# Optimization experiments

Measured on AMD Instinct MI355X. Metric: run time of the kernel, lower is better.

Reference implementation:

```python
import jax, jax.numpy as jnp
import numpy as np

GRID_SIZE = 64
THRESHOLD = 1.0
SIGMA = 1.5
K_SHARP = 2.0


def _gaussian_kernel(sigma):
    ksize = max(int(4 * sigma) | 1, 3)
    x = jnp.arange(ksize, dtype=jnp.float32) - ksize // 2
    g1d = jnp.exp(-x ** 2 / (2.0 * sigma ** 2))
    g2d = g1d[None, :] * g1d[:, None]
    g2d = g2d / g2d.sum()
    return g2d[None, None]  # (1,1,k,k) OIHW


def setup_inputs() -> dict:
    key = jax.random.key(0)
    k1, k2, k3, k4 = jax.random.split(key, 4)
    B, V, P, N, MAXP = 4, 512, 8192, 2000, 8
    positions = jax.random.uniform(k1, (B, V, 2), dtype=jnp.float32) * 2.0 - 1.0
    pin_offsets = jax.random.normal(k2, (P, 2), dtype=jnp.float32) * 0.05
    net_to_pin = jax.random.randint(k3, (N, MAXP), 0, P, dtype=jnp.int32)
    pin_to_macro = jax.random.randint(k4, (P,), 0, V, dtype=jnp.int32)
    return {"positions": positions, "pin_offsets": pin_offsets,
            "net_to_pin": net_to_pin, "pin_to_macro": pin_to_macro}


def reference(positions, pin_offsets, net_to_pin, pin_to_macro):
    B = positions.shape[0]
    M = GRID_SIZE
    num_nets = net_to_pin.shape[0]

    # pin positions: (B, P, 2) -- no rotation (rotation_onehot=None branch)
    pin_pos = positions[:, pin_to_macro, :] + pin_offsets[None]

    # per-net bounding boxes over valid pins
    valid = net_to_pin >= 0                                  # (N, maxp)
    safe_idx = jnp.maximum(net_to_pin, 0)
    net_pin_pos = pin_pos[:, safe_idx, :]                    # (B, N, maxp, 2)
    mask = valid[None, :, :, None]
    bbox_max = jnp.max(jnp.where(mask, net_pin_pos, -1e9), axis=2)  # (B, N, 2)
    bbox_min = jnp.min(jnp.where(mask, net_pin_pos, 1e9), axis=2)

    # to grid coordinates
    bbox_max_g = (bbox_max + 1.0) * 0.5 * (M - 1)
    bbox_min_g = (bbox_min + 1.0) * 0.5 * (M - 1)

    # soft rectangular indicators on the MxM grid
    gx = jnp.arange(M, dtype=jnp.float32)
    grid_x, grid_y = jnp.meshgrid(gx, gx, indexing="xy")     # (M, M)
    grid_x = grid_x[None, None]                               # (1,1,M,M)
    grid_y = grid_y[None, None]
    x_min = bbox_min_g[..., 0][..., None, None]               # (B,N,1,1)
    x_max = bbox_max_g[..., 0][..., None, None]
    y_min = bbox_min_g[..., 1][..., None, None]
    y_max = bbox_max_g[..., 1][..., None, None]

    in_x = jax.nn.sigmoid(K_SHARP * (grid_x - x_min + 0.5)) * \
           jax.nn.sigmoid(K_SHARP * (x_max - grid_x + 0.5))
    in_y = jax.nn.sigmoid(K_SHARP * (grid_y - y_min + 0.5)) * \
           jax.nn.sigmoid(K_SHARP * (y_max - grid_y + 0.5))
    indicator = in_x * in_y                                    # (B,N,M,M)

    bbox_size = jnp.maximum((x_max - x_min + 1.0) * (y_max - y_min + 1.0), 1.0)
    rudy = jnp.sum(indicator / bbox_size, axis=1, keepdims=True)  # (B,1,M,M)

    # gaussian smoothing (SAME padding)
    kernel = _gaussian_kernel(SIGMA)
    pad = kernel.shape[-1] // 2
    rudy_smooth = jax.lax.conv_general_dilated(
        rudy, kernel, window_strides=(1, 1),
        padding=((pad, pad), (pad, pad)),
        dimension_numbers=("NCHW", "OIHW", "NCHW"))

    overflow = jax.nn.relu(rudy_smooth - THRESHOLD)
    penalty = jnp.sum(overflow ** 2, axis=(1, 2, 3))           # (B,)
    return penalty, rudy_smooth
```

## Files before the change

kernel.cpp:

```cpp
#include <hip/hip_runtime.h>

#define GRID   64
#define CELLS  (GRID * GRID)
#define BATCH  4
#define NV     512
#define NNET   2000
#define MAXPIN 8
#define NB     32
#define NPART  63

__device__ __forceinline__ float sig2(float a, float b) {
    float e1 = __expf(-a);
    float e2 = __expf(-b);
    return 1.0f / ((1.0f + e1) * (1.0f + e2));
}

__global__ __launch_bounds__(512)
void rudy_partial_kernel(const float* __restrict__ positions,
                         const float* __restrict__ pin_offsets,
                         const int*   __restrict__ net_to_pin,
                         const int*   __restrict__ pin_to_macro,
                         float* __restrict__ partial,
                         float* __restrict__ out_penalty) {
    const int pb = blockIdx.x;
    const int b  = blockIdx.y;
    const int t  = threadIdx.x;

    if (pb == 0 && t == 0) out_penalty[b] = 0.0f;

    __shared__ float s_inx[NB][GRID];
    __shared__ float s_iny[NB][GRID];
    __shared__ float s_xmin[NB], s_xmax[NB], s_ymin[NB], s_ymax[NB], s_inv[NB];

    const int n0 = pb * NB;

    if (t < 256) {
        const int nl = t >> 3;
        const int j  = t & 7;
        const int n  = n0 + nl;
        int pi = (n < NNET) ? net_to_pin[n * MAXPIN + j] : -1;
        int sp = pi > 0 ? pi : 0;
        int v  = pin_to_macro[sp];
        float px = positions[(b * NV + v) * 2 + 0] + pin_offsets[sp * 2 + 0];
        float py = positions[(b * NV + v) * 2 + 1] + pin_offsets[sp * 2 + 1];
        bool valid = pi >= 0;
        float xmx = valid ? px : -1e9f;
        float xmn = valid ? px :  1e9f;
        float ymx = valid ? py : -1e9f;
        float ymn = valid ? py :  1e9f;
        #pragma unroll
        for (int off = 1; off < 8; off <<= 1) {
            xmx = fmaxf(xmx, __shfl_xor(xmx, off, 64));
            xmn = fminf(xmn, __shfl_xor(xmn, off, 64));
            ymx = fmaxf(ymx, __shfl_xor(ymx, off, 64));
            ymn = fminf(ymn, __shfl_xor(ymn, off, 64));
        }
        if (j == 0) {
            float xming = (xmn + 1.0f) * 31.5f;
            float xmaxg = (xmx + 1.0f) * 31.5f;
            float yming = (ymn + 1.0f) * 31.5f;
            float ymaxg = (ymx + 1.0f) * 31.5f;
            float size = fmaxf((xmaxg - xming + 1.0f) * (ymaxg - yming + 1.0f), 1.0f);
            s_xmin[nl] = xming; s_xmax[nl] = xmaxg;
            s_ymin[nl] = yming; s_ymax[nl] = ymaxg;
            s_inv[nl]  = 1.0f / size;
        }
    }
    __syncthreads();

    #pragma unroll
    for (int i = 0; i < 8; ++i) {
        int vv    = i * 512 + t;
        int n     = vv >> 7;
        int rem   = vv & 127;
        int which = rem >> 6;
        int coord = rem & 63;
        float c  = (float)coord;
        float lo = which ? s_ymin[n] : s_xmin[n];
        float hi = which ? s_ymax[n] : s_xmax[n];
        float val = sig2(2.0f * (c - lo + 0.5f), 2.0f * (hi - c + 0.5f));
        if (which) s_iny[n][coord] = val;
        else       s_inx[n][coord] = val * s_inv[n];
    }
    __syncthreads();

    const int lane = t & 63;
    const int w    = t >> 6;
    float acc[8];
    #pragma unroll
    for (int k = 0; k < 8; ++k) acc[k] = 0.0f;

    for (int n = 0; n < NB; ++n) {
        float xv = s_inx[n][lane];
        const float4* iny4 = (const float4*)&s_iny[n][w * 8];
        #pragma unroll
        for (int k4 = 0; k4 < 2; ++k4) {
            float4 yv = iny4[k4];
            acc[k4 * 4 + 0] += yv.x * xv;
            acc[k4 * 4 + 1] += yv.y * xv;
            acc[k4 * 4 + 2] += yv.z * xv;
            acc[k4 * 4 + 3] += yv.w * xv;
        }
    }

    float* dst = partial + ((size_t)b * NPART + pb) * CELLS;
    #pragma unroll
    for (int k = 0; k < 8; ++k)
        dst[(w * 8 + k) * GRID + lane] = acc[k];
}

#define SROWS 14
__global__ __launch_bounds__(256)
void reduce_smooth_penalty_kernel(const float* __restrict__ partial,
                                  float* __restrict__ out_penalty,
                                  float* __restrict__ out_smooth) {
    const int q = blockIdx.x;
    const int b = blockIdx.y;
    const int t = threadIdx.x;
    const int y0 = q * 8;

    __shared__ float tile[SROWS][GRID];
    __shared__ float tmp [SROWS][GRID];
    __shared__ float red [4];

    float g[7];
    {
        float s = 0.0f;
        #pragma unroll
        for (int i = 0; i < 7; ++i) {
            float d = (float)(i - 3);
            g[i] = expf(-d * d / 4.5f);
            s += g[i];
        }
        float inv = 1.0f / s;
        #pragma unroll
        for (int i = 0; i < 7; ++i) g[i] *= inv;
    }

    if (t < SROWS * 16) {
        const int r  = t >> 4;
        const int c4 = t & 15;
        const int yy = y0 - 3 + r;
        float4 a0 = {0,0,0,0}, a1 = {0,0,0,0}, a2 = {0,0,0,0}, a3 = {0,0,0,0};
        if (yy >= 0 && yy < GRID) {
            const float4* src = (const float4*)(partial + (size_t)b * NPART * CELLS)
                                + (size_t)yy * 16 + c4;
            int p = 0;
            for (; p + 3 < NPART; p += 4) {
                float4 v0 = src[(size_t)(p + 0) * (CELLS / 4)];
                float4 v1 = src[(size_t)(p + 1) * (CELLS / 4)];
                float4 v2 = src[(size_t)(p + 2) * (CELLS / 4)];
                float4 v3 = src[(size_t)(p + 3) * (CELLS / 4)];
                a0.x += v0.x; a0.y += v0.y; a0.z += v0.z; a0.w += v0.w;
                a1.x += v1.x; a1.y += v1.y; a1.z += v1.z; a1.w += v1.w;
                a2.x += v2.x; a2.y += v2.y; a2.z += v2.z; a2.w += v2.w;
                a3.x += v3.x; a3.y += v3.y; a3.z += v3.z; a3.w += v3.w;
            }
            for (; p < NPART; ++p) {
                float4 v0 = src[(size_t)p * (CELLS / 4)];
                a0.x += v0.x; a0.y += v0.y; a0.z += v0.z; a0.w += v0.w;
            }
            a0.x += a1.x + a2.x + a3.x;
            a0.y += a1.y + a2.y + a3.y;
            a0.z += a1.z + a2.z + a3.z;
            a0.w += a1.w + a2.w + a3.w;
        }
        ((float4*)&tile[r][0])[c4] = a0;
    }
    __syncthreads();

    for (int i = t; i < SROWS * GRID; i += 256) {
        int r = i >> 6, x = i & 63;
        float s = 0.0f;
        #pragma unroll
        for (int d = -3; d <= 3; ++d) {
            int xx = x + d;
            if (xx >= 0 && xx < GRID) s += g[d + 3] * tile[r][xx];
        }
        tmp[r][x] = s;
    }
    __syncthreads();

    float local = 0.0f;
    #pragma unroll
    for (int i = 0; i < 2; ++i) {
        int c = i * 256 + t;
        int r = c >> 6, x = c & 63;
        float s = 0.0f;
        #pragma unroll
        for (int d = -3; d <= 3; ++d)
            s += g[d + 3] * tmp[r + 3 + d][x];
        out_smooth[b * CELLS + (y0 + r) * GRID + x] = s;
        float ov = s - 1.0f;
        ov = ov > 0.0f ? ov : 0.0f;
        local += ov * ov;
    }

    #pragma unroll
    for (int off = 32; off > 0; off >>= 1) local += __shfl_down(local, off, 64);
    if ((t & 63) == 0) red[t >> 6] = local;
    __syncthreads();
    if (t == 0)
        atomicAdd(&out_penalty[b], red[0] + red[1] + red[2] + red[3]);
}

extern "C" void kernel_launch(void* const* d_in, const int* in_sizes, int n_in,
                              void* d_out, int out_size, void* d_ws, size_t ws_size,
                              hipStream_t stream) {
    const float* positions    = (const float*)d_in[0];
    const float* pin_offsets  = (const float*)d_in[1];
    const int*   net_to_pin   = (const int*)d_in[2];
    const int*   pin_to_macro = (const int*)d_in[3];
    float* out     = (float*)d_out;
    float* partial = (float*)d_ws;

    rudy_partial_kernel<<<dim3(NPART, BATCH), 512, 0, stream>>>(
        positions, pin_offsets, net_to_pin, pin_to_macro, partial, out);
    reduce_smooth_penalty_kernel<<<dim3(8, BATCH), 256, 0, stream>>>(
        partial, out, out + BATCH);
}
```

Measured before the change: 74.65 us.

## Fuse partial-RUDY and reduce/smooth kernels with atomic counter handoff

Merges the two kernels into one launch. Extra blocks spin on a per-batch atomic counter until all partial blocks have published their results, then reduce, smooth and compute the penalty. The final penalty is written by the last slice through a second counter instead of float atomicAdd. This removes one kernel launch and the gap between kernels, but adds a memset launch and spin-waiting blocks that rely on the partial blocks being scheduled, which is a forward-progress risk.

After: 139.7 us. 1.87x slower.

```diff
diff --git a/kernel.cpp b/kernel.cpp
--- a/kernel.cpp
+++ b/kernel.cpp
@@ -8,6 +8,14 @@
 #define MAXPIN 8
 #define NB     32
 #define NPART  63
+#define NSLICE 8
+#define SROWS  14
+
+struct SyncBlock {
+    int   cnt1[BATCH];
+    int   cnt2[BATCH];
+    float pen[BATCH][NSLICE];
+};
 
 __device__ __forceinline__ float sig2(float a, float b) {
     float e1 = __expf(-a);
@@ -16,112 +24,125 @@
 }
 
 __global__ __launch_bounds__(512)
-void rudy_partial_kernel(const float* __restrict__ positions,
-                         const float* __restrict__ pin_offsets,
-                         const int*   __restrict__ net_to_pin,
-                         const int*   __restrict__ pin_to_macro,
-                         float* __restrict__ partial,
-                         float* __restrict__ out_penalty) {
+void rudy_fused_kernel(const float* __restrict__ positions,
+                       const float* __restrict__ pin_offsets,
+                       const int*   __restrict__ net_to_pin,
+                       const int*   __restrict__ pin_to_macro,
+                       float* __restrict__ partial,
+                       SyncBlock*   __restrict__ sync,
+                       float* __restrict__ out_penalty,
+                       float* __restrict__ out_smooth) {
     const int pb = blockIdx.x;
     const int b  = blockIdx.y;
     const int t  = threadIdx.x;
 
-    if (pb == 0 && t == 0) out_penalty[b] = 0.0f;
-
-    __shared__ float s_inx[NB][GRID];
-    __shared__ float s_iny[NB][GRID];
-    __shared__ float s_xmin[NB], s_xmax[NB], s_ymin[NB], s_ymax[NB], s_inv[NB];
-
-    const int n0 = pb * NB;
-
-    if (t < 256) {
-        const int nl = t >> 3;
-        const int j  = t & 7;
-        const int n  = n0 + nl;
-        int pi = (n < NNET) ? net_to_pin[n * MAXPIN + j] : -1;
-        int sp = pi > 0 ? pi : 0;
-        int v  = pin_to_macro[sp];
-        float px = positions[(b * NV + v) * 2 + 0] + pin_offsets[sp * 2 + 0];
-        float py = positions[(b * NV + v) * 2 + 1] + pin_offsets[sp * 2 + 1];
-        bool valid = pi >= 0;
-        float xmx = valid ? px : -1e9f;
-        float xmn = valid ? px :  1e9f;
-        float ymx = valid ? py : -1e9f;
-        float ymn = valid ? py :  1e9f;
-        #pragma unroll
-        for (int off = 1; off < 8; off <<= 1) {
-            xmx = fmaxf(xmx, __shfl_xor(xmx, off, 64));
-            xmn = fminf(xmn, __shfl_xor(xmn, off, 64));
-            ymx = fmaxf(ymx, __shfl_xor(ymx, off, 64));
-            ymn = fminf(ymn, __shfl_xor(ymn, off, 64));
-        }
-        if (j == 0) {
-            float xming = (xmn + 1.0f) * 31.5f;
-            float xmaxg = (xmx + 1.0f) * 31.5f;
-            float yming = (ymn + 1.0f) * 31.5f;
-            float ymaxg = (ymx + 1.0f) * 31.5f;
-            float size = fmaxf((xmaxg - xming + 1.0f) * (ymaxg - yming + 1.0f), 1.0f);
-            s_xmin[nl] = xming; s_xmax[nl] = xmaxg;
-            s_ymin[nl] = yming; s_ymax[nl] = ymaxg;
-            s_inv[nl]  = 1.0f / size;
-        }
-    }
-    __syncthreads();
-
-    #pragma unroll
-    for (int i = 0; i < 8; ++i) {
-        int vv    = i * 512 + t;
-        int n     = vv >> 7;
-        int rem   = vv & 127;
-        int which = rem >> 6;
-        int coord = rem & 63;
-        float c  = (float)coord;
-        float lo = which ? s_ymin[n] : s_xmin[n];
-        float hi = which ? s_ymax[n] : s_xmax[n];
-        float val = sig2(2.0f * (c - lo + 0.5f), 2.0f * (hi - c + 0.5f));
-        if (which) s_iny[n][coord] = val;
-        else       s_inx[n][coord] = val * s_inv[n];
-    }
-    __syncthreads();
-
-    const int lane = t & 63;
-    const int w    = t >> 6;
-    float acc[8];
-    #pragma unroll
-    for (int k = 0; k < 8; ++k) acc[k] = 0.0f;
-
-    for (int n = 0; n < NB; ++n) {
-        float xv = s_inx[n][lane];
-        const float4* iny4 = (const float4*)&s_iny[n][w * 8];
-        #pragma unroll
-        for (int k4 = 0; k4 < 2; ++k4) {
-            float4 yv = iny4[k4];
-            acc[k4 * 4 + 0] += yv.x * xv;
-            acc[k4 * 4 + 1] += yv.y * xv;
-            acc[k4 * 4 + 2] += yv.z * xv;
-            acc[k4 * 4 + 3] += yv.w * xv;
-        }
-    }
-
-    float* dst = partial + ((size_t)b * NPART + pb) * CELLS;
-    #pragma unroll
-    for (int k = 0; k < 8; ++k)
-        dst[(w * 8 + k) * GRID + lane] = acc[k];
-}
-
-#define SROWS 14
-__global__ __launch_bounds__(256)
-void reduce_smooth_penalty_kernel(const float* __restrict__ partial,
-                                  float* __restrict__ out_penalty,
-                                  float* __restrict__ out_smooth) {
-    const int q = blockIdx.x;
-    const int b = blockIdx.y;
-    const int t = threadIdx.x;
+    __shared__ union {
+        struct {
+            float inx[NB][GRID];
+            float iny[NB][GRID];
+            float xmin[NB], xmax[NB], ymin[NB], ymax[NB], inv[NB];
+        } a;
+        struct {
+            float tile[SROWS][GRID];
+            float tmp [SROWS][GRID];
+            float red [8];
+        } s;
+    } sm;
+
+    if (pb < NPART) {
+        const int n0 = pb * NB;
+
+        if (t < 256) {
+            const int nl = t >> 3;
+            const int j  = t & 7;
+            const int n  = n0 + nl;
+            int pi = (n < NNET) ? net_to_pin[n * MAXPIN + j] : -1;
+            int sp = pi > 0 ? pi : 0;
+            int v  = pin_to_macro[sp];
+            float px = positions[(b * NV + v) * 2 + 0] + pin_offsets[sp * 2 + 0];
+            float py = positions[(b * NV + v) * 2 + 1] + pin_offsets[sp * 2 + 1];
+            bool valid = pi >= 0;
+            float xmx = valid ? px : -1e9f;
+            float xmn = valid ? px :  1e9f;
+            float ymx = valid ? py : -1e9f;
+            float ymn = valid ? py :  1e9f;
+            #pragma unroll
+            for (int off = 1; off < 8; off <<= 1) {
+                xmx = fmaxf(xmx, __shfl_xor(xmx, off, 64));
+                xmn = fminf(xmn, __shfl_xor(xmn, off, 64));
+                ymx = fmaxf(ymx, __shfl_xor(ymx, off, 64));
+                ymn = fminf(ymn, __shfl_xor(ymn, off, 64));
+            }
+            if (j == 0) {
+                float xming = (xmn + 1.0f) * 31.5f;
+                float xmaxg = (xmx + 1.0f) * 31.5f;
+                float yming = (ymn + 1.0f) * 31.5f;
+                float ymaxg = (ymx + 1.0f) * 31.5f;
+                float size = fmaxf((xmaxg - xming + 1.0f) * (ymaxg - yming + 1.0f), 1.0f);
+                sm.a.xmin[nl] = xming; sm.a.xmax[nl] = xmaxg;
+                sm.a.ymin[nl] = yming; sm.a.ymax[nl] = ymaxg;
+                sm.a.inv[nl]  = 1.0f / size;
+            }
+        }
+        __syncthreads();
+
+        #pragma unroll
+        for (int i = 0; i < 8; ++i) {
+            int vv    = i * 512 + t;
+            int n     = vv >> 7;
+            int rem   = vv & 127;
+            int which = rem >> 6;
+            int coord = rem & 63;
+            float c  = (float)coord;
+            float lo = which ? sm.a.ymin[n] : sm.a.xmin[n];
+            float hi = which ? sm.a.ymax[n] : sm.a.xmax[n];
+            float val = sig2(2.0f * (c - lo + 0.5f), 2.0f * (hi - c + 0.5f));
+            if (which) sm.a.iny[n][coord] = val;
+            else       sm.a.inx[n][coord] = val * sm.a.inv[n];
+        }
+        __syncthreads();
+
+        const int lane = t & 63;
+        const int w    = t >> 6;
+        float acc[8];
+        #pragma unroll
+        for (int k = 0; k < 8; ++k) acc[k] = 0.0f;
+
+        for (int n = 0; n < NB; ++n) {
+            float xv = sm.a.inx[n][lane];
+            const float4* iny4 = (const float4*)&sm.a.iny[n][w * 8];
+            #pragma unroll
+            for (int k4 = 0; k4 < 2; ++k4) {
+                float4 yv = iny4[k4];
+                acc[k4 * 4 + 0] += yv.x * xv;
+                acc[k4 * 4 + 1] += yv.y * xv;
+                acc[k4 * 4 + 2] += yv.z * xv;
+                acc[k4 * 4 + 3] += yv.w * xv;
+            }
+        }
+
+        float* dst = partial + ((size_t)b * NPART + pb) * CELLS;
+        #pragma unroll
+        for (int k = 0; k < 8; ++k)
+            dst[(w * 8 + k) * GRID + lane] = acc[k];
+
+        __threadfence();
+        __syncthreads();
+        if (t == 0)
+            __hip_atomic_fetch_add(&sync->cnt1[b], 1,
+                                   __ATOMIC_RELEASE, __HIP_MEMORY_SCOPE_AGENT);
+        return;
+    }
+
+    const int q  = pb - NPART;
     const int y0 = q * 8;
 
-    __shared__ float tile[SROWS][GRID];
-    __shared__ float tmp [SROWS][GRID];
-    __shared__ float red [4];
+    if (t == 0) {
+        while (__hip_atomic_load(&sync->cnt1[b],
+                                 __ATOMIC_ACQUIRE, __HIP_MEMORY_SCOPE_AGENT) < NPART)
+            __builtin_amdgcn_s_sleep(2);
+    }
+    __syncthreads();
 
     float g[7];
     {
@@ -165,43 +186,57 @@
             a0.z += a1.z + a2.z + a3.z;
             a0.w += a1.w + a2.w + a3.w;
         }
-        ((float4*)&tile[r][0])[c4] = a0;
-    }
-    __syncthreads();
-
-    for (int i = t; i < SROWS * GRID; i += 256) {
+        ((float4*)&sm.s.tile[r][0])[c4] = a0;
+    }
+    __syncthreads();
+
+    for (int i = t; i < SROWS * GRID; i += 512) {
         int r = i >> 6, x = i & 63;
         float s = 0.0f;
         #pragma unroll
         for (int d = -3; d <= 3; ++d) {
             int xx = x + d;
-            if (xx >= 0 && xx < GRID) s += g[d + 3] * tile[r][xx];
-        }
-        tmp[r][x] = s;
-    }
-    __syncthreads();
-
-    float local = 0.0f;
-    #pragma unroll
-    for (int i = 0; i < 2; ++i) {
-        int c = i * 256 + t;
-        int r = c >> 6, x = c & 63;
+            if (xx >= 0 && xx < GRID) s += g[d + 3] * sm.s.tile[r][xx];
+        }
+        sm.s.tmp[r][x] = s;
+    }
+    __syncthreads();
+
+    float local;
+    {
+        int r = t >> 6, x = t & 63;
         float s = 0.0f;
         #pragma unroll
         for (int d = -3; d <= 3; ++d)
-            s += g[d + 3] * tmp[r + 3 + d][x];
+            s += g[d + 3] * sm.s.tmp[r + 3 + d][x];
         out_smooth[b * CELLS + (y0 + r) * GRID + x] = s;
         float ov = s - 1.0f;
         ov = ov > 0.0f ? ov : 0.0f;
-        local += ov * ov;
+        local = ov * ov;
     }
 
     #pragma unroll
     for (int off = 32; off > 0; off >>= 1) local += __shfl_down(local, off, 64);
-    if ((t & 63) == 0) red[t >> 6] = local;
-    __syncthreads();
-    if (t == 0)
-        atomicAdd(&out_penalty[b], red[0] + red[1] + red[2] + red[3]);
+    if ((t & 63) == 0) sm.s.red[t >> 6] = local;
+    __syncthreads();
+
+    if (t == 0) {
+        float share = 0.0f;
+        #pragma unroll
+        for (int i = 0; i < 8; ++i) share += sm.s.red[i];
+        __hip_atomic_store(&sync->pen[b][q], share,
+                           __ATOMIC_RELEASE, __HIP_MEMORY_SCOPE_AGENT);
+        int r = __hip_atomic_fetch_add(&sync->cnt2[b], 1,
+                                       __ATOMIC_ACQ_REL, __HIP_MEMORY_SCOPE_AGENT);
+        if (r == NSLICE - 1) {
+            float s = 0.0f;
+            #pragma unroll
+            for (int i = 0; i < NSLICE; ++i)
+                s += __hip_atomic_load(&sync->pen[b][i],
+                                       __ATOMIC_ACQUIRE, __HIP_MEMORY_SCOPE_AGENT);
+            out_penalty[b] = s;
+        }
+    }
 }
 
 extern "C" void kernel_launch(void* const* d_in, const int* in_sizes, int n_in,
@@ -213,9 +248,10 @@
     const int*   pin_to_macro = (const int*)d_in[3];
     float* out     = (float*)d_out;
     float* partial = (float*)d_ws;
-
-    rudy_partial_kernel<<<dim3(NPART, BATCH), 512, 0, stream>>>(
-        positions, pin_offsets, net_to_pin, pin_to_macro, partial, out);
-    reduce_smooth_penalty_kernel<<<dim3(8, BATCH), 256, 0, stream>>>(
-        partial, out, out + BATCH);
+    SyncBlock* sync = (SyncBlock*)(partial + (size_t)BATCH * NPART * CELLS);
+
+    hipMemsetAsync(sync, 0, sizeof(SyncBlock), stream);
+    rudy_fused_kernel<<<dim3(NPART + NSLICE, BATCH), 512, 0, stream>>>(
+        positions, pin_offsets, net_to_pin, pin_to_macro,
+        partial, sync, out, out + BATCH);
 }
```
